# Kernel optimization log

Hardware: AMD Instinct MI355X
Metric: run time of the kernel (lower is better)

The kernel has to match this reference:

```python
import jax, jax.numpy as jnp
import numpy as np


def setup_inputs() -> dict:
    key = jax.random.key(0)
    k1, k2 = jax.random.split(key)
    B, Sx, Sy, D = 8, 2048, 2048, 1024
    x = jax.random.normal(k1, (B, Sx, D), dtype=jnp.float32)
    y = jax.random.normal(k2, (B, Sy, D), dtype=jnp.float32)
    return {"x": x, "y": y}


def reference(x, y):
    # e[b,i,j] = x[b,i,:] . y[b,j,:]  (UNscaled, as in the original)
    e = jnp.einsum('bid,bjd->bij', x, y)
    ai = jax.nn.softmax(e, axis=-1)
    # a[b,i,:] = sum_j ai[b,i,j] * y[b,j,:]
    a = jnp.einsum('bij,bjd->bid', ai, y)
    # concat along feature dim; dropout p=0 -> identity
    out = jnp.concatenate([x, a], axis=-1)  # [B, Sx, 2D]
    return out
```

## Files before the change

kernel.cpp:

```cpp
#include <hip/hip_runtime.h>
#include <stdint.h>

#define SX 2048
#define SYY 2048
#define DDIM 1024
#define NBATCH 8

typedef _Float16 f16;
typedef __attribute__((ext_vector_type(2))) _Float16 h2_t;
typedef __attribute__((ext_vector_type(4))) _Float16 h4_t;
typedef __attribute__((ext_vector_type(8))) _Float16 h8_t;
typedef __attribute__((ext_vector_type(4))) float fx4_t;

__device__ __forceinline__ void gload_lds16(const void* g, void* l) {
  __builtin_amdgcn_global_load_lds((const __attribute__((address_space(1))) void*)g,
                                   (__attribute__((address_space(3))) void*)l,
                                   16, 0, 0);
}

__global__ __launch_bounds__(256) void k_prep_x(const float4* __restrict__ x,
                                                float* __restrict__ out,
                                                h4_t* __restrict__ x16, long n4) {
  long i = (long)blockIdx.x * blockDim.x + threadIdx.x;
  long stride = (long)gridDim.x * blockDim.x;
  for (; i < n4; i += stride) {
    long bi = i >> 8;
    int dq = (int)(i & 255);
    float4 v = x[i];
    *(float4*)(out + bi * (2 * DDIM) + dq * 4) = v;
    h4_t h = { (f16)v.x, (f16)v.y, (f16)v.z, (f16)v.w };
    x16[i] = h;
  }
}

__global__ __launch_bounds__(256) void k_trans(const float* __restrict__ y,
                                               f16* __restrict__ y16,
                                               f16* __restrict__ yt16) {
  __shared__ f16 tile[64][72];
  int z = blockIdx.z;
  int d0 = blockIdx.x * 64, j0 = blockIdx.y * 64;
  const float* yb = y + (size_t)z * SYY * DDIM;
  f16* y16b = y16 + (size_t)z * SYY * DDIM;
  f16* ytb = yt16 + (size_t)z * DDIM * SYY;
  int t = threadIdx.x;
  int jl = t >> 2;
  int dq = t & 3;
#pragma unroll
  for (int s = 0; s < 4; ++s) {
    int dl = dq * 16 + s * 4;
    float4 v = *(const float4*)(yb + (size_t)(j0 + jl) * DDIM + d0 + dl);
    h4_t h = { (f16)v.x, (f16)v.y, (f16)v.z, (f16)v.w };
    *(h4_t*)(y16b + (size_t)(j0 + jl) * DDIM + d0 + dl) = h;
    *(h4_t*)&tile[jl][dl] = h;
  }
  __syncthreads();
  int dl2 = t >> 2;
  int jq = t & 3;
  f16 vbuf[16] __attribute__((aligned(16)));
#pragma unroll
  for (int u = 0; u < 16; ++u) vbuf[u] = tile[jq * 16 + u][dl2];
  f16* orow = ytb + (size_t)(d0 + dl2) * SYY + j0 + jq * 16;
  *(uint4*)orow = *(const uint4*)&vbuf[0];
  *(uint4*)(orow + 8) = *(const uint4*)&vbuf[8];
}

#define PH_BAR() __builtin_amdgcn_s_barrier()

#define STAGE_A(SLOT, HALF, T) {                                               \
    const f16* s_ = aRow + (size_t)((HALF) * 64) * lda + (T) * 64;             \
    f16* d_ = lds + (SLOT) * 8192 + dstoff;                                    \
    gload_lds16(s_, d_);                                                       \
    gload_lds16(s_ + (size_t)128 * lda, d_ + 4096); }

#define STAGE_B(SLOT, HALF, T) {                                               \
    const f16* s_ = bRow + (size_t)((HALF) * 32) * ldb + (T) * 64;             \
    f16* d_ = lds + (SLOT) * 8192 + dstoff;                                    \
    gload_lds16(s_, d_);                                                       \
    gload_lds16(s_ + (size_t)128 * ldb, d_ + 4096); }

#define RD_A(PTR, CB) { _Pragma("unroll") for (int i_ = 0; i_ < 4; ++i_) {     \
    af[i_][0] = *(const h8_t*)((PTR) + (CB) + i_ * 2048 + kb0);                \
    af[i_][1] = *(const h8_t*)((PTR) + (CB) + i_ * 2048 + kb1); } }

#define RD_A_S(PTR, CB, MOFF) { _Pragma("unroll") for (int i_ = 0; i_ < 4; ++i_) { \
    h8_t a0 = *(const h8_t*)((PTR) + (CB) + i_ * 2048 + kb0);                  \
    h8_t a1 = *(const h8_t*)((PTR) + (CB) + i_ * 2048 + kb1);                  \
    h2_t* p0 = (h2_t*)&a0; h2_t* p1 = (h2_t*)&a1;                              \
    _Pragma("unroll") for (int q_ = 0; q_ < 4; ++q_) {                         \
      p0[q_] *= fdc[(MOFF) + i_]; p1[q_] *= fdc[(MOFF) + i_]; }                \
    af[i_][0] = a0; af[i_][1] = a1; } }

#define RD_B(PTR, CB, NH) { _Pragma("unroll") for (int j_ = 0; j_ < 2; ++j_) { \
    bf[(NH) + j_][0] = *(const h8_t*)((PTR) + (CB) + j_ * 2048 + kb0);         \
    bf[(NH) + j_][1] = *(const h8_t*)((PTR) + (CB) + j_ * 2048 + kb1); } }

#define MM(MH, NH) { __builtin_amdgcn_s_setprio(1);                            \
  _Pragma("unroll") for (int i_ = 0; i_ < 4; ++i_)                             \
  _Pragma("unroll") for (int j_ = 0; j_ < 2; ++j_) {                           \
    acc[(MH) + i_][(NH) + j_] = __builtin_amdgcn_mfma_f32_16x16x32_f16(        \
        af[i_][0], bf[(NH) + j_][0], acc[(MH) + i_][(NH) + j_], 0, 0, 0);      \
    acc[(MH) + i_][(NH) + j_] = __builtin_amdgcn_mfma_f32_16x16x32_f16(        \
        af[i_][1], bf[(NH) + j_][1], acc[(MH) + i_][(NH) + j_], 0, 0, 0); }    \
  __builtin_amdgcn_s_setprio(0); }

#define DECODE_TILE()                                                          \
  int bid = blockIdx.x;                                                        \
  int id = bid;                                                                \
  if ((nblk & 7) == 0) { int cpx = nblk >> 3; id = (bid & 7) * cpx + (bid >> 3); } \
  int tpz = ntm * ntn;                                                         \
  int z = id / tpz;                                                            \
  int rem = id - z * tpz;                                                      \
  int mt, ntl;                                                                 \
  if ((ntm & 1) == 0) {                                                        \
    int ht = tpz >> 1, hm = ntm >> 1;                                          \
    int half = rem / ht, j = rem - half * ht;                                  \
    ntl = j / hm; mt = half * hm + (j - ntl * hm);                             \
  } else { mt = rem / ntn; ntl = rem - mt * ntn; }                             \
  int m0 = mt * 256, n0 = ntl * 256;

#define GEMM_COMMON_SETUP()                                                    \
  const int tid = threadIdx.x;                                                 \
  const int lane = tid & 63, w = tid >> 6;                                     \
  const int wr = w >> 2, wc = w & 3;                                           \
  const int fr = lane & 15, fh = lane >> 4;                                    \
  const f16* Ab = A + (size_t)z * a_zs + (size_t)(a_row0 + m0) * lda;          \
  const f16* Bb = B + (size_t)z * b_zs + (size_t)n0 * ldb;                     \
  const int l0 = 8 * w + (lane >> 3);                                          \
  const int r0a = l0;                                                          \
  const int r0b = ((l0 >> 5) << 6) | (l0 & 31);                                \
  const int swz = 8 * ((lane & 7) ^ (lane >> 3));                              \
  const f16* aRow = Ab + (size_t)r0a * lda + swz;                              \
  const f16* bRow = Bb + (size_t)r0b * ldb + swz;                              \
  const int dstoff = w * 512 + lane * 8;                                       \
  const char* ldsAlo = (const char*)lds + wr * 8192 + fr * 128;                \
  const char* ldsAhi = ldsAlo + 16384;                                         \
  const char* ldsBlo = (const char*)lds + 32768 + wc * 4096 + fr * 128;        \
  const char* ldsBhi = ldsBlo + 16384;                                         \
  const int kb0 = ((0 + fh) ^ (fr & 7)) * 16;                                  \
  const int kb1 = ((4 + fh) ^ (fr & 7)) * 16;

__global__ __launch_bounds__(512, 2) void k_gemm1(
    const f16* __restrict__ A, long a_zs, int a_row0, int lda,
    const f16* __restrict__ B, long b_zs, int ldb,
    f16* __restrict__ U, long u_zs,
    float2* __restrict__ ML, int mrows,
    int K, int ntm, int ntn, int nblk)
{
  __shared__ f16 lds[65536];
  DECODE_TILE();
  GEMM_COMMON_SETUP();

  const int nt = K >> 6;
  const int ng = nt >> 1;

  fx4_t acc[8][4];
#pragma unroll
  for (int i = 0; i < 8; ++i)
#pragma unroll
    for (int j = 0; j < 4; ++j) { fx4_t zv = {0.f,0.f,0.f,0.f}; acc[i][j] = zv; }
  h8_t af[4][2], bf[4][2];

  STAGE_A(0, 0, 0); STAGE_A(1, 1, 0); STAGE_B(2, 0, 0); STAGE_B(3, 1, 0);
  STAGE_A(4, 0, 1); STAGE_B(6, 0, 1); STAGE_B(7, 1, 1);
  asm volatile("s_waitcnt vmcnt(6)" ::: "memory");
  PH_BAR();

  for (int g = 0; g < ng; ++g) {
    const int T1 = 2 * g + 1, T2 = 2 * g + 2, T3 = 2 * g + 3;
    const bool nl = (g < ng - 1);
    RD_A(ldsAlo, 0); RD_B(ldsBlo, 0, 0);
    STAGE_A(5, 1, T1);
    PH_BAR();
    MM(0, 0);
    PH_BAR();
    RD_B(ldsBhi, 0, 2);
    if (nl) STAGE_A(0, 0, T2);
    PH_BAR();
    MM(0, 2);
    PH_BAR();
    RD_A(ldsAhi, 0);
    if (nl) STAGE_B(2, 0, T2);
    PH_BAR();
    MM(4, 0);
    PH_BAR();
    if (nl) STAGE_B(3, 1, T2);
    PH_BAR();
    MM(4, 2);
    if (nl) { asm volatile("s_waitcnt vmcnt(6)" ::: "memory"); }
    else    { asm volatile("s_waitcnt vmcnt(0)" ::: "memory"); }
    PH_BAR();
    RD_A(ldsAlo, 65536); RD_B(ldsBlo, 65536, 0);
    if (nl) STAGE_A(1, 1, T2);
    PH_BAR();
    MM(0, 0);
    PH_BAR();
    RD_B(ldsBhi, 65536, 2);
    if (nl) STAGE_A(4, 0, T3);
    PH_BAR();
    MM(0, 2);
    PH_BAR();
    RD_A(ldsAhi, 65536);
    if (nl) STAGE_B(6, 0, T3);
    PH_BAR();
    MM(4, 0);
    PH_BAR();
    if (nl) STAGE_B(7, 1, T3);
    PH_BAR();
    MM(4, 2);
    asm volatile("s_waitcnt vmcnt(6)" ::: "memory");
    PH_BAR();
  }

  __syncthreads();
  float* red = (float*)lds;
  const int rbase = wr * 128 + fh * 4;
  float pm[8][4];
#pragma unroll
  for (int mi = 0; mi < 8; ++mi)
#pragma unroll
    for (int rr = 0; rr < 4; ++rr)
      pm[mi][rr] = fmaxf(fmaxf(acc[mi][0][rr], acc[mi][1][rr]),
                         fmaxf(acc[mi][2][rr], acc[mi][3][rr]));
#pragma unroll
  for (int off = 8; off > 0; off >>= 1)
#pragma unroll
    for (int mi = 0; mi < 8; ++mi)
#pragma unroll
      for (int rr = 0; rr < 4; ++rr)
        pm[mi][rr] = fmaxf(pm[mi][rr], __shfl_xor(pm[mi][rr], off));
  if (fr == 0)
#pragma unroll
    for (int mi = 0; mi < 8; ++mi)
#pragma unroll
      for (int rr = 0; rr < 4; ++rr)
        red[wc * 256 + rbase + mi * 16 + rr] = pm[mi][rr];
  __syncthreads();
  float mrow[8][4];
#pragma unroll
  for (int mi = 0; mi < 8; ++mi)
#pragma unroll
    for (int rr = 0; rr < 4; ++rr) {
      int r = rbase + mi * 16 + rr;
      mrow[mi][rr] = fmaxf(fmaxf(red[r], red[256 + r]),
                           fmaxf(red[512 + r], red[768 + r]));
    }
  __syncthreads();
  float ps[8][4];
#pragma unroll
  for (int mi = 0; mi < 8; ++mi)
#pragma unroll
    for (int rr = 0; rr < 4; ++rr) {
      float s = 0.f;
#pragma unroll
      for (int ni = 0; ni < 4; ++ni) {
        float e = __expf(acc[mi][ni][rr] - mrow[mi][rr]);
        acc[mi][ni][rr] = e;
        s += e;
      }
      ps[mi][rr] = s;
    }
#pragma unroll
  for (int off = 8; off > 0; off >>= 1)
#pragma unroll
    for (int mi = 0; mi < 8; ++mi)
#pragma unroll
      for (int rr = 0; rr < 4; ++rr)
        ps[mi][rr] += __shfl_xor(ps[mi][rr], off);
  if (fr == 0)
#pragma unroll
    for (int mi = 0; mi < 8; ++mi)
#pragma unroll
      for (int rr = 0; rr < 4; ++rr)
        red[wc * 256 + rbase + mi * 16 + rr] = ps[mi][rr];
  __syncthreads();
  f16* Ub = U + (size_t)z * u_zs;
#pragma unroll
  for (int mi = 0; mi < 8; ++mi)
#pragma unroll
    for (int ni = 0; ni < 4; ++ni)
#pragma unroll
      for (int rr = 0; rr < 4; ++rr)
        Ub[(size_t)(m0 + rbase + mi * 16 + rr) * SYY +
           n0 + wc * 64 + ni * 16 + fr] = (f16)acc[mi][ni][rr];
  if (wc == 0 && fr == 0) {
    float2* MLp = ML + ((size_t)z * 8 + ntl) * mrows + m0;
#pragma unroll
    for (int mi = 0; mi < 8; ++mi)
#pragma unroll
      for (int rr = 0; rr < 4; ++rr) {
        int r = rbase + mi * 16 + rr;
        float l4 = red[r] + red[256 + r] + red[512 + r] + red[768 + r];
        float2 v; v.x = mrow[mi][rr]; v.y = l4;
        MLp[r] = v;
      }
  }
}

__global__ __launch_bounds__(256) void k_mlred(const float2* __restrict__ ML,
                                               f16* __restrict__ Fq,
                                               int rows, long total) {
  long idx = (long)blockIdx.x * blockDim.x + threadIdx.x;
  if (idx >= total) return;
  int z = (int)(idx / rows);
  int r = (int)(idx - (long)z * rows);
  float2 v[8];
  float M = -3.4e38f;
#pragma unroll
  for (int t = 0; t < 8; ++t) {
    v[t] = ML[((size_t)z * 8 + t) * rows + r];
    M = fmaxf(M, v[t].x);
  }
  float L = 0.f;
#pragma unroll
  for (int t = 0; t < 8; ++t) L += v[t].y * __expf(v[t].x - M);
  float inv = 1.0f / L;
#pragma unroll
  for (int t = 0; t < 8; ++t)
    Fq[((size_t)z * 8 + t) * rows + r] = (f16)(__expf(v[t].x - M) * inv);
}

__global__ __launch_bounds__(512, 2) void k_gemm2(
    const f16* __restrict__ A, long a_zs, int a_row0, int lda,
    const f16* __restrict__ B, long b_zs, int ldb,
    float* __restrict__ C, long c_zs, int c_row0, int ldc, int c_col0,
    const f16* __restrict__ Fq, int mrows,
    int K, int ntm, int ntn, int nblk)
{
  __shared__ f16 lds[65536];
  DECODE_TILE();
  GEMM_COMMON_SETUP();

  const int nt = K >> 6;
  const int ng = nt >> 1;

  fx4_t acc[8][4];
#pragma unroll
  for (int i = 0; i < 8; ++i)
#pragma unroll
    for (int j = 0; j < 4; ++j) { fx4_t zv = {0.f,0.f,0.f,0.f}; acc[i][j] = zv; }
  h8_t af[4][2], bf[4][2];

  const f16* Fb = Fq + (size_t)z * 8 * mrows + m0 + wr * 128 + fr;
  h2_t fdc[8], fdn[8];
#pragma unroll
  for (int i = 0; i < 8; ++i) {
    f16 fv = Fb[i * 16];
    h2_t d; d[0] = fv; d[1] = fv; fdn[i] = d;
  }

  STAGE_A(0, 0, 0); STAGE_A(1, 1, 0); STAGE_B(2, 0, 0); STAGE_B(3, 1, 0);
  STAGE_A(4, 0, 1); STAGE_B(6, 0, 1); STAGE_B(7, 1, 1);
  asm volatile("s_waitcnt vmcnt(6)" ::: "memory");
  PH_BAR();

  for (int g = 0; g < ng; ++g) {
    const int T1 = 2 * g + 1, T2 = 2 * g + 2, T3 = 2 * g + 3;
    const bool nl = (g < ng - 1);
    if ((g & 1) == 0) {
#pragma unroll
      for (int i = 0; i < 8; ++i) fdc[i] = fdn[i];
      int tn = (g >> 1) + 1;
      if (tn < 8) {
        const f16* Fn = Fb + (size_t)tn * mrows;
#pragma unroll
        for (int i = 0; i < 8; ++i) {
          f16 fv = Fn[i * 16];
          h2_t d; d[0] = fv; d[1] = fv; fdn[i] = d;
        }
      }
    }
    RD_A_S(ldsAlo, 0, 0); RD_B(ldsBlo, 0, 0);
    STAGE_A(5, 1, T1);
    PH_BAR();
    MM(0, 0);
    PH_BAR();
    RD_B(ldsBhi, 0, 2);
    if (nl) STAGE_A(0, 0, T2);
    PH_BAR();
    MM(0, 2);
    PH_BAR();
    RD_A_S(ldsAhi, 0, 4);
    if (nl) STAGE_B(2, 0, T2);
    PH_BAR();
    MM(4, 0);
    PH_BAR();
    if (nl) STAGE_B(3, 1, T2);
    PH_BAR();
    MM(4, 2);
    if (nl) { asm volatile("s_waitcnt vmcnt(6)" ::: "memory"); }
    else    { asm volatile("s_waitcnt vmcnt(0)" ::: "memory"); }
    PH_BAR();
    RD_A_S(ldsAlo, 65536, 0); RD_B(ldsBlo, 65536, 0);
    if (nl) STAGE_A(1, 1, T2);
    PH_BAR();
    MM(0, 0);
    PH_BAR();
    RD_B(ldsBhi, 65536, 2);
    if (nl) STAGE_A(4, 0, T3);
    PH_BAR();
    MM(0, 2);
    PH_BAR();
    RD_A_S(ldsAhi, 65536, 4);
    if (nl) STAGE_B(6, 0, T3);
    PH_BAR();
    MM(4, 0);
    PH_BAR();
    if (nl) STAGE_B(7, 1, T3);
    PH_BAR();
    MM(4, 2);
    asm volatile("s_waitcnt vmcnt(6)" ::: "memory");
    PH_BAR();
  }

  float* Cb = C + (size_t)z * c_zs +
              (size_t)(c_row0 + m0 + wr * 128) * ldc + c_col0 + n0 + wc * 64;
#pragma unroll
  for (int mi = 0; mi < 8; ++mi)
#pragma unroll
    for (int ni = 0; ni < 4; ++ni)
#pragma unroll
      for (int r = 0; r < 4; ++r)
        Cb[(size_t)(mi * 16 + fh * 4 + r) * ldc + ni * 16 + fr] = acc[mi][ni][r];
}

extern "C" void kernel_launch(void* const* d_in, const int* in_sizes, int n_in,
                              void* d_out, int out_size, void* d_ws, size_t ws_size,
                              hipStream_t stream) {
  (void)in_sizes; (void)n_in; (void)out_size;
  const float* x = (const float*)d_in[0];
  const float* y = (const float*)d_in[1];
  float* out = (float*)d_out;

  size_t per_batch = (size_t)SX * SYY * 2 + (size_t)8 * SX * 8 + (size_t)8 * SX * 2 +
                     (size_t)SX * DDIM * 2 + (size_t)SYY * DDIM * 2 +
                     (size_t)DDIM * SYY * 2;
  int nb = (int)(ws_size / per_batch);
  if (nb > NBATCH) nb = NBATCH;
  int CH = SX;
  if (nb < 1) {
    nb = 1;
    size_t conv = (size_t)SX * DDIM * 2 + (size_t)SYY * DDIM * 2 +
                  (size_t)DDIM * SYY * 2;
    size_t avail = ws_size > conv ? ws_size - conv : 0;
    long ch = (long)(avail / ((size_t)SYY * 2 + 80));
    ch = (ch / 256) * 256;
    if (ch < 256) ch = 256;
    if (ch > SX) ch = SX;
    CH = (int)ch;
  }

  char* w = (char*)d_ws;
  f16* Ubuf = (f16*)w;            size_t off = (size_t)nb * CH * SYY * 2;
  float2* MLbuf = (float2*)(w + off); off += (size_t)nb * 8 * CH * 8;
  f16* Fqbuf = (f16*)(w + off);   off += (size_t)nb * 8 * CH * 2;
  f16* X16 = (f16*)(w + off);     off += (size_t)nb * SX * DDIM * 2;
  f16* Y16 = (f16*)(w + off);     off += (size_t)nb * SYY * DDIM * 2;
  f16* Yt16 = (f16*)(w + off);

  for (int b0 = 0; b0 < NBATCH; b0 += nb) {
    int nbc = (NBATCH - b0 < nb) ? (NBATCH - b0) : nb;
    k_prep_x<<<2048, 256, 0, stream>>>(
        (const float4*)(x + (size_t)b0 * SX * DDIM),
        out + (size_t)b0 * SX * 2 * DDIM, (h4_t*)X16,
        (long)nbc * SX * (DDIM / 4));
    dim3 tg(DDIM / 64, SYY / 64, nbc);
    k_trans<<<tg, 256, 0, stream>>>(y + (size_t)b0 * SYY * DDIM, Y16, Yt16);

    for (int i0 = 0; i0 < SX; i0 += CH) {
      int ntm = CH / 256;
      int nblk1 = nbc * ntm * (SYY / 256);
      k_gemm1<<<nblk1, 512, 0, stream>>>(X16, (long)SX * DDIM, i0, DDIM,
                                         Y16, (long)SYY * DDIM, DDIM,
                                         Ubuf, (long)CH * SYY,
                                         MLbuf, CH,
                                         DDIM, ntm, SYY / 256, nblk1);
      long rows_total = (long)nbc * CH;
      k_mlred<<<(unsigned)((rows_total + 255) / 256), 256, 0, stream>>>(
          MLbuf, Fqbuf, CH, rows_total);
      int nblk2 = nbc * ntm * (DDIM / 256);
      k_gemm2<<<nblk2, 512, 0, stream>>>(Ubuf, (long)CH * SYY, 0, SYY,
                                         Yt16, (long)DDIM * SYY, SYY,
                                         out + (size_t)b0 * SX * 2 * DDIM,
                                         (long)SX * 2 * DDIM, i0, 2 * DDIM, DDIM,
                                         Fqbuf, CH,
                                         SYY, ntm, DDIM / 256, nblk2);
    }
  }
}
```

Baseline: 221.0 us.

## Process two tiles per gemm1 block, prefetching the next tile during epilogue

k_gemm1 now launches half as many blocks, each computing two output tiles back to back. The global-to-LDS staging for the second tile starts while the first tile's last k-steps and softmax epilogue run, so the prologue and epilogue are hidden inside one continuous pipeline. The epilogue is also restructured: the per-row max and sum are found with in-wave shuffles and one LDS exchange in a separate region, replacing several __syncthreads rounds. In k_gemm2 the scale-factor prefetch load moves to mid-iteration. The costs are larger LDS, more index arithmetic, fewer blocks to spread across CUs, and a more complex pipeline.

```diff
diff --git a/kernel.cpp b/kernel.cpp
--- a/kernel.cpp
+++ b/kernel.cpp
@@ -66,14 +66,14 @@
 
 #define PH_BAR() __builtin_amdgcn_s_barrier()
 
-#define STAGE_A(SLOT, HALF, T) {                                               \
-    const f16* s_ = aRow + (size_t)((HALF) * 64) * lda + (T) * 64;             \
+#define STAGE_A(AR, SLOT, HALF, T) {                                           \
+    const f16* s_ = (AR) + (size_t)((HALF) * 64) * lda + (T) * 64;             \
     f16* d_ = lds + (SLOT) * 8192 + dstoff;                                    \
     gload_lds16(s_, d_);                                                       \
     gload_lds16(s_ + (size_t)128 * lda, d_ + 4096); }
 
-#define STAGE_B(SLOT, HALF, T) {                                               \
-    const f16* s_ = bRow + (size_t)((HALF) * 32) * ldb + (T) * 64;             \
+#define STAGE_B(BR, SLOT, HALF, T) {                                           \
+    const f16* s_ = (BR) + (size_t)((HALF) * 32) * ldb + (T) * 64;             \
     f16* d_ = lds + (SLOT) * 8192 + dstoff;                                    \
     gload_lds16(s_, d_);                                                       \
     gload_lds16(s_ + (size_t)128 * ldb, d_ + 4096); }
@@ -103,34 +103,14 @@
         af[i_][1], bf[(NH) + j_][1], acc[(MH) + i_][(NH) + j_], 0, 0, 0); }    \
   __builtin_amdgcn_s_setprio(0); }
 
-#define DECODE_TILE()                                                          \
-  int bid = blockIdx.x;                                                        \
-  int id = bid;                                                                \
-  if ((nblk & 7) == 0) { int cpx = nblk >> 3; id = (bid & 7) * cpx + (bid >> 3); } \
-  int tpz = ntm * ntn;                                                         \
-  int z = id / tpz;                                                            \
-  int rem = id - z * tpz;                                                      \
-  int mt, ntl;                                                                 \
-  if ((ntm & 1) == 0) {                                                        \
-    int ht = tpz >> 1, hm = ntm >> 1;                                          \
-    int half = rem / ht, j = rem - half * ht;                                  \
-    ntl = j / hm; mt = half * hm + (j - ntl * hm);                             \
-  } else { mt = rem / ntn; ntl = rem - mt * ntn; }                             \
-  int m0 = mt * 256, n0 = ntl * 256;
-
 #define GEMM_COMMON_SETUP()                                                    \
   const int tid = threadIdx.x;                                                 \
   const int lane = tid & 63, w = tid >> 6;                                     \
   const int wr = w >> 2, wc = w & 3;                                           \
   const int fr = lane & 15, fh = lane >> 4;                                    \
-  const f16* Ab = A + (size_t)z * a_zs + (size_t)(a_row0 + m0) * lda;          \
-  const f16* Bb = B + (size_t)z * b_zs + (size_t)n0 * ldb;                     \
   const int l0 = 8 * w + (lane >> 3);                                          \
-  const int r0a = l0;                                                          \
   const int r0b = ((l0 >> 5) << 6) | (l0 & 31);                                \
   const int swz = 8 * ((lane & 7) ^ (lane >> 3));                              \
-  const f16* aRow = Ab + (size_t)r0a * lda + swz;                              \
-  const f16* bRow = Bb + (size_t)r0b * ldb + swz;                              \
   const int dstoff = w * 512 + lane * 8;                                       \
   const char* ldsAlo = (const char*)lds + wr * 8192 + fr * 128;                \
   const char* ldsAhi = ldsAlo + 16384;                                         \
@@ -139,19 +119,44 @@
   const int kb0 = ((0 + fh) ^ (fr & 7)) * 16;                                  \
   const int kb1 = ((4 + fh) ^ (fr & 7)) * 16;
 
+#define COMPUTE_TILE(IDX, AR, BR, ZV, M0V, N0V) {                              \
+    int id_ = (IDX);                                                           \
+    ZV = id_ / tpz; int rem_ = id_ - ZV * tpz;                                 \
+    int mt_, ntl_;                                                             \
+    if ((ntm & 1) == 0) {                                                      \
+      int ht_ = tpz >> 1, hm_ = ntm >> 1;                                      \
+      int half_ = rem_ / ht_, j_ = rem_ - half_ * ht_;                         \
+      ntl_ = j_ / hm_; mt_ = half_ * hm_ + (j_ - ntl_ * hm_);                  \
+    } else { mt_ = rem_ / ntn; ntl_ = rem_ - mt_ * ntn; }                      \
+    M0V = mt_ * 256; N0V = ntl_ * 256;                                         \
+    AR = A + (size_t)ZV * a_zs + (size_t)(a_row0 + M0V) * lda                  \
+           + (size_t)l0 * lda + swz;                                           \
+    BR = B + (size_t)ZV * b_zs + (size_t)N0V * ldb                             \
+           + (size_t)r0b * ldb + swz; }
+
 __global__ __launch_bounds__(512, 2) void k_gemm1(
     const f16* __restrict__ A, long a_zs, int a_row0, int lda,
     const f16* __restrict__ B, long b_zs, int ldb,
     f16* __restrict__ U, long u_zs,
     float2* __restrict__ ML, int mrows,
-    int K, int ntm, int ntn, int nblk)
+    int K, int ntm, int ntn, int nblk, int tpb)
 {
-  __shared__ f16 lds[65536];
-  DECODE_TILE();
+  __shared__ f16 lds[69632];
   GEMM_COMMON_SETUP();
-
+  const int tpz = ntm * ntn;
   const int nt = K >> 6;
   const int ng = nt >> 1;
+  const int nphys = nblk / tpb;
+  const int nper = nblk >> 3, bper = nphys >> 3;
+  const int xcd = blockIdx.x & 7, lb = blockIdx.x >> 3;
+  const bool chunk8 = ((nblk & 7) == 0) && ((nphys & 7) == 0);
+
+  const f16 *aRowC, *bRowC, *aRowN = A, *bRowN = B;
+  int zC, m0C, n0C, zN = 0, m0N = 0, n0N = 0;
+  int id0 = chunk8 ? (xcd * nper + lb) : (int)blockIdx.x;
+  int idstep = chunk8 ? bper : nphys;
+  COMPUTE_TILE(id0, aRowC, bRowC, zC, m0C, n0C);
+  if (tpb > 1) COMPUTE_TILE(id0 + idstep, aRowN, bRowN, zN, m0N, n0N);
 
   fx4_t acc[8][4];
 #pragma unroll
@@ -160,139 +165,108 @@
     for (int j = 0; j < 4; ++j) { fx4_t zv = {0.f,0.f,0.f,0.f}; acc[i][j] = zv; }
   h8_t af[4][2], bf[4][2];
 
-  STAGE_A(0, 0, 0); STAGE_A(1, 1, 0); STAGE_B(2, 0, 0); STAGE_B(3, 1, 0);
-  STAGE_A(4, 0, 1); STAGE_B(6, 0, 1); STAGE_B(7, 1, 1);
+  STAGE_A(aRowC, 0, 0, 0); STAGE_A(aRowC, 1, 1, 0);
+  STAGE_B(bRowC, 2, 0, 0); STAGE_B(bRowC, 3, 1, 0);
+  STAGE_A(aRowC, 4, 0, 1); STAGE_B(bRowC, 6, 0, 1); STAGE_B(bRowC, 7, 1, 1);
   asm volatile("s_waitcnt vmcnt(6)" ::: "memory");
   PH_BAR();
 
-  for (int g = 0; g < ng; ++g) {
-    const int T1 = 2 * g + 1, T2 = 2 * g + 2, T3 = 2 * g + 3;
-    const bool nl = (g < ng - 1);
+  const int GG = ng * tpb, KT = nt * tpb;
+  int tl = 0;
+  for (int gg = 0; gg < GG; ++gg) {
+    const int gloc = gg - tl * ng;
+    const int T1 = 2 * gloc + 1;
+    const int kt2 = 2 * gg + 2, kt3 = 2 * gg + 3;
+    const bool h2 = kt2 < KT, h3 = kt3 < KT;
+    const int tb = (tl + 1) * nt;
+    const bool n2 = kt2 >= tb, n3 = kt3 >= tb;
+    const f16* a2 = n2 ? aRowN : aRowC; const f16* b2 = n2 ? bRowN : bRowC;
+    const f16* a3 = n3 ? aRowN : aRowC; const f16* b3 = n3 ? bRowN : bRowC;
+    const int T2 = kt2 - (n2 ? tb : tl * nt);
+    const int T3 = kt3 - (n3 ? tb : tl * nt);
     RD_A(ldsAlo, 0); RD_B(ldsBlo, 0, 0);
-    STAGE_A(5, 1, T1);
-    PH_BAR();
-    MM(0, 0);
-    PH_BAR();
+    STAGE_A(aRowC, 5, 1, T1);
+    PH_BAR(); MM(0, 0); PH_BAR();
     RD_B(ldsBhi, 0, 2);
-    if (nl) STAGE_A(0, 0, T2);
-    PH_BAR();
-    MM(0, 2);
-    PH_BAR();
+    if (h2) STAGE_A(a2, 0, 0, T2);
+    PH_BAR(); MM(0, 2); PH_BAR();
     RD_A(ldsAhi, 0);
-    if (nl) STAGE_B(2, 0, T2);
-    PH_BAR();
-    MM(4, 0);
-    PH_BAR();
-    if (nl) STAGE_B(3, 1, T2);
-    PH_BAR();
-    MM(4, 2);
-    if (nl) { asm volatile("s_waitcnt vmcnt(6)" ::: "memory"); }
+    if (h2) STAGE_B(b2, 2, 0, T2);
+    PH_BAR(); MM(4, 0); PH_BAR();
+    if (h2) STAGE_B(b2, 3, 1, T2);
+    PH_BAR(); MM(4, 2);
+    if (h2) { asm volatile("s_waitcnt vmcnt(6)" ::: "memory"); }
     else    { asm volatile("s_waitcnt vmcnt(0)" ::: "memory"); }
     PH_BAR();
     RD_A(ldsAlo, 65536); RD_B(ldsBlo, 65536, 0);
-    if (nl) STAGE_A(1, 1, T2);
+    if (h2) STAGE_A(a2, 1, 1, T2);
+    PH_BAR(); MM(0, 0); PH_BAR();
+    RD_B(ldsBhi, 65536, 2);
+    if (h3) STAGE_A(a3, 4, 0, T3);
+    PH_BAR(); MM(0, 2); PH_BAR();
+    RD_A(ldsAhi, 65536);
+    if (h3) STAGE_B(b3, 6, 0, T3);
+    PH_BAR(); MM(4, 0); PH_BAR();
+    if (h3) STAGE_B(b3, 7, 1, T3);
+    PH_BAR(); MM(4, 2);
+    if (h2) { asm volatile("s_waitcnt vmcnt(6)" ::: "memory"); }
+    else    { asm volatile("s_waitcnt vmcnt(0)" ::: "memory"); }
     PH_BAR();
-    MM(0, 0);
-    PH_BAR();
-    RD_B(ldsBhi, 65536, 2);
-    if (nl) STAGE_A(4, 0, T3);
-    PH_BAR();
-    MM(0, 2);
-    PH_BAR();
-    RD_A(ldsAhi, 65536);
-    if (nl) STAGE_B(6, 0, T3);
-    PH_BAR();
-    MM(4, 0);
-    PH_BAR();
-    if (nl) STAGE_B(7, 1, T3);
-    PH_BAR();
-    MM(4, 2);
-    asm volatile("s_waitcnt vmcnt(6)" ::: "memory");
-    PH_BAR();
-  }
-
-  __syncthreads();
-  float* red = (float*)lds;
-  const int rbase = wr * 128 + fh * 4;
-  float pm[8][4];
-#pragma unroll
-  for (int mi = 0; mi < 8; ++mi)
-#pragma unroll
-    for (int rr = 0; rr < 4; ++rr)
-      pm[mi][rr] = fmaxf(fmaxf(acc[mi][0][rr], acc[mi][1][rr]),
-                         fmaxf(acc[mi][2][rr], acc[mi][3][rr]));
-#pragma unroll
-  for (int off = 8; off > 0; off >>= 1)
-#pragma unroll
-    for (int mi = 0; mi < 8; ++mi)
-#pragma unroll
-      for (int rr = 0; rr < 4; ++rr)
-        pm[mi][rr] = fmaxf(pm[mi][rr], __shfl_xor(pm[mi][rr], off));
-  if (fr == 0)
-#pragma unroll
-    for (int mi = 0; mi < 8; ++mi)
-#pragma unroll
-      for (int rr = 0; rr < 4; ++rr)
-        red[wc * 256 + rbase + mi * 16 + rr] = pm[mi][rr];
-  __syncthreads();
-  float mrow[8][4];
-#pragma unroll
-  for (int mi = 0; mi < 8; ++mi)
-#pragma unroll
-    for (int rr = 0; rr < 4; ++rr) {
-      int r = rbase + mi * 16 + rr;
-      mrow[mi][rr] = fmaxf(fmaxf(red[r], red[256 + r]),
-                           fmaxf(red[512 + r], red[768 + r]));
+
+    if (gloc == ng - 1) {
+      float2* mlx = (float2*)(lds + 65536);
+      const int rbase = wr * 128 + fh * 4;
+      float mw[8][4];
+#pragma unroll
+      for (int mi = 0; mi < 8; ++mi)
+#pragma unroll
+        for (int rr = 0; rr < 4; ++rr) {
+          float am = fmaxf(fmaxf(acc[mi][0][rr], acc[mi][1][rr]),
+                           fmaxf(acc[mi][2][rr], acc[mi][3][rr]));
+          am = fmaxf(am, __shfl_xor(am, 1)); am = fmaxf(am, __shfl_xor(am, 2));
+          am = fmaxf(am, __shfl_xor(am, 4)); am = fmaxf(am, __shfl_xor(am, 8));
+          float s = 0.f;
+#pragma unroll
+          for (int ni = 0; ni < 4; ++ni) {
+            float e = __expf(acc[mi][ni][rr] - am);
+            acc[mi][ni][rr] = e; s += e;
+          }
+          s += __shfl_xor(s, 1); s += __shfl_xor(s, 2);
+          s += __shfl_xor(s, 4); s += __shfl_xor(s, 8);
+          mw[mi][rr] = am;
+          if (fr == 0) {
+            float2 v; v.x = am; v.y = s;
+            mlx[(rbase + mi * 16 + rr) * 4 + wc] = v;
+          }
+        }
+      asm volatile("s_waitcnt lgkmcnt(0)" ::: "memory");
+      PH_BAR();
+      f16* Ub = U + (size_t)zC * u_zs;
+      float2* MLp = ML + ((size_t)zC * 8 + (n0C >> 8)) * mrows + m0C;
+#pragma unroll
+      for (int mi = 0; mi < 8; ++mi)
+#pragma unroll
+        for (int rr = 0; rr < 4; ++rr) {
+          int row = rbase + mi * 16 + rr;
+          float4 p01 = *(float4*)&mlx[row * 4 + 0];
+          float4 p23 = *(float4*)&mlx[row * 4 + 2];
+          float mt = fmaxf(fmaxf(p01.x, p01.z), fmaxf(p23.x, p23.z));
+          float lt = p01.y * __expf(p01.x - mt) + p01.w * __expf(p01.z - mt) +
+                     p23.y * __expf(p23.x - mt) + p23.w * __expf(p23.z - mt);
+          float sc = __expf(mw[mi][rr] - mt);
+#pragma unroll
+          for (int ni = 0; ni < 4; ++ni)
+            Ub[(size_t)(m0C + row) * SYY + n0C + wc * 64 + ni * 16 + fr] =
+                (f16)(acc[mi][ni][rr] * sc);
+          if (wc == 0 && fr == 0) { float2 v; v.x = mt; v.y = lt; MLp[row] = v; }
+        }
+      aRowC = aRowN; bRowC = bRowN; zC = zN; m0C = m0N; n0C = n0N;
+      ++tl;
+#pragma unroll
+      for (int i = 0; i < 8; ++i)
+#pragma unroll
+        for (int j = 0; j < 4; ++j) { fx4_t zv = {0.f,0.f,0.f,0.f}; acc[i][j] = zv; }
     }
-  __syncthreads();
-  float ps[8][4];
-#pragma unroll
-  for (int mi = 0; mi < 8; ++mi)
-#pragma unroll
-    for (int rr = 0; rr < 4; ++rr) {
-      float s = 0.f;
-#pragma unroll
-      for (int ni = 0; ni < 4; ++ni) {
-        float e = __expf(acc[mi][ni][rr] - mrow[mi][rr]);
-        acc[mi][ni][rr] = e;
-        s += e;
-      }
-      ps[mi][rr] = s;
-    }
-#pragma unroll
-  for (int off = 8; off > 0; off >>= 1)
-#pragma unroll
-    for (int mi = 0; mi < 8; ++mi)
-#pragma unroll
-      for (int rr = 0; rr < 4; ++rr)
-        ps[mi][rr] += __shfl_xor(ps[mi][rr], off);
-  if (fr == 0)
-#pragma unroll
-    for (int mi = 0; mi < 8; ++mi)
-#pragma unroll
-      for (int rr = 0; rr < 4; ++rr)
-        red[wc * 256 + rbase + mi * 16 + rr] = ps[mi][rr];
-  __syncthreads();
-  f16* Ub = U + (size_t)z * u_zs;
-#pragma unroll
-  for (int mi = 0; mi < 8; ++mi)
-#pragma unroll
-    for (int ni = 0; ni < 4; ++ni)
-#pragma unroll
-      for (int rr = 0; rr < 4; ++rr)
-        Ub[(size_t)(m0 + rbase + mi * 16 + rr) * SYY +
-           n0 + wc * 64 + ni * 16 + fr] = (f16)acc[mi][ni][rr];
-  if (wc == 0 && fr == 0) {
-    float2* MLp = ML + ((size_t)z * 8 + ntl) * mrows + m0;
-#pragma unroll
-    for (int mi = 0; mi < 8; ++mi)
-#pragma unroll
-      for (int rr = 0; rr < 4; ++rr) {
-        int r = rbase + mi * 16 + rr;
-        float l4 = red[r] + red[256 + r] + red[512 + r] + red[768 + r];
-        float2 v; v.x = mrow[mi][rr]; v.y = l4;
-        MLp[r] = v;
-      }
   }
 }
 
@@ -327,8 +301,14 @@
     int K, int ntm, int ntn, int nblk)
 {
   __shared__ f16 lds[65536];
-  DECODE_TILE();
   GEMM_COMMON_SETUP();
+  const int tpz = ntm * ntn;
+  int bid = blockIdx.x;
+  int id = bid;
+  if ((nblk & 7) == 0) { int cpx = nblk >> 3; id = (bid & 7) * cpx + (bid >> 3); }
+  const f16 *aRow, *bRow;
+  int z, m0, n0;
+  COMPUTE_TILE(id, aRow, bRow, z, m0, n0);
 
   const int nt = K >> 6;
   const int ng = nt >> 1;
@@ -348,17 +328,36 @@
     h2_t d; d[0] = fv; d[1] = fv; fdn[i] = d;
   }
 
-  STAGE_A(0, 0, 0); STAGE_A(1, 1, 0); STAGE_B(2, 0, 0); STAGE_B(3, 1, 0);
-  STAGE_A(4, 0, 1); STAGE_B(6, 0, 1); STAGE_B(7, 1, 1);
+  STAGE_A(aRow, 0, 0, 0); STAGE_A(aRow, 1, 1, 0);
+  STAGE_B(bRow, 2, 0, 0); STAGE_B(bRow, 3, 1, 0);
+  STAGE_A(aRow, 4, 0, 1); STAGE_B(bRow, 6, 0, 1); STAGE_B(bRow, 7, 1, 1);
   asm volatile("s_waitcnt vmcnt(6)" ::: "memory");
   PH_BAR();
 
   for (int g = 0; g < ng; ++g) {
     const int T1 = 2 * g + 1, T2 = 2 * g + 2, T3 = 2 * g + 3;
     const bool nl = (g < ng - 1);
-    if ((g & 1) == 0) {
+    const bool ev = ((g & 1) == 0);
+    if (ev) {
 #pragma unroll
       for (int i = 0; i < 8; ++i) fdc[i] = fdn[i];
+    }
+    RD_A_S(ldsAlo, 0, 0); RD_B(ldsBlo, 0, 0);
+    STAGE_A(aRow, 5, 1, T1);
+    PH_BAR(); MM(0, 0); PH_BAR();
+    RD_B(ldsBhi, 0, 2);
+    if (nl) STAGE_A(aRow, 0, 0, T2);
+    PH_BAR(); MM(0, 2); PH_BAR();
+    RD_A_S(ldsAhi, 0, 4);
+    if (nl) STAGE_B(bRow, 2, 0, T2);
+    PH_BAR(); MM(4, 0); PH_BAR();
+    if (nl) STAGE_B(bRow, 3, 1, T2);
+    PH_BAR(); MM(4, 2);
+    if (nl) { asm volatile("s_waitcnt vmcnt(6)" ::: "memory"); }
+    else    { asm volatile("s_waitcnt vmcnt(0)" ::: "memory"); }
+    PH_BAR();
+    RD_A_S(ldsAlo, 65536, 0); RD_B(ldsBlo, 65536, 0);
+    if (ev) {
       int tn = (g >> 1) + 1;
       if (tn < 8) {
         const f16* Fn = Fb + (size_t)tn * mrows;
@@ -369,45 +368,16 @@
         }
       }
     }
-    RD_A_S(ldsAlo, 0, 0); RD_B(ldsBlo, 0, 0);
-    STAGE_A(5, 1, T1);
-    PH_BAR();
-    MM(0, 0);
-    PH_BAR();
-    RD_B(ldsBhi, 0, 2);
-    if (nl) STAGE_A(0, 0, T2);
-    PH_BAR();
-    MM(0, 2);
-    PH_BAR();
-    RD_A_S(ldsAhi, 0, 4);
-    if (nl) STAGE_B(2, 0, T2);
-    PH_BAR();
-    MM(4, 0);
-    PH_BAR();
-    if (nl) STAGE_B(3, 1, T2);
-    PH_BAR();
-    MM(4, 2);
-    if (nl) { asm volatile("s_waitcnt vmcnt(6)" ::: "memory"); }
-    else    { asm volatile("s_waitcnt vmcnt(0)" ::: "memory"); }
-    PH_BAR();
-    RD_A_S(ldsAlo, 65536, 0); RD_B(ldsBlo, 65536, 0);
-    if (nl) STAGE_A(1, 1, T2);
-    PH_BAR();
-    MM(0, 0);
-    PH_BAR();
+    if (nl) STAGE_A(aRow, 1, 1, T2);
+    PH_BAR(); MM(0, 0); PH_BAR();
     RD_B(ldsBhi, 65536, 2);
-    if (nl) STAGE_A(4, 0, T3);
-    PH_BAR();
-    MM(0, 2);
-    PH_BAR();
+    if (nl) STAGE_A(aRow, 4, 0, T3);
+    PH_BAR(); MM(0, 2); PH_BAR();
     RD_A_S(ldsAhi, 65536, 4);
-    if (nl) STAGE_B(6, 0, T3);
-    PH_BAR();
-    MM(4, 0);
-    PH_BAR();
-    if (nl) STAGE_B(7, 1, T3);
-    PH_BAR();
-    MM(4, 2);
+    if (nl) STAGE_B(bRow, 6, 0, T3);
+    PH_BAR(); MM(4, 0); PH_BAR();
+    if (nl) STAGE_B(bRow, 7, 1, T3);
+    PH_BAR(); MM(4, 2);
     asm volatile("s_waitcnt vmcnt(6)" ::: "memory");
     PH_BAR();
   }
@@ -469,11 +439,13 @@
     for (int i0 = 0; i0 < SX; i0 += CH) {
       int ntm = CH / 256;
       int nblk1 = nbc * ntm * (SYY / 256);
-      k_gemm1<<<nblk1, 512, 0, stream>>>(X16, (long)SX * DDIM, i0, DDIM,
-                                         Y16, (long)SYY * DDIM, DDIM,
-                                         Ubuf, (long)CH * SYY,
-                                         MLbuf, CH,
-                                         DDIM, ntm, SYY / 256, nblk1);
+      int tpb = ((nblk1 & 15) == 0) ? 2 : 1;
+      int nphys1 = nblk1 / tpb;
+      k_gemm1<<<nphys1, 512, 0, stream>>>(X16, (long)SX * DDIM, i0, DDIM,
+                                          Y16, (long)SYY * DDIM, DDIM,
+                                          Ubuf, (long)CH * SYY,
+                                          MLbuf, CH,
+                                          DDIM, ntm, SYY / 256, nblk1, tpb);
       long rows_total = (long)nbc * CH;
       k_mlred<<<(unsigned)((rows_total + 255) / 256), 256, 0, stream>>>(
           MLbuf, Fqbuf, CH, rows_total);
```

Measured after the change: 235.5 us. 1.07x slower.

## Fuse softmax max/sum reductions per wave and coalesce U stores via LDS

Applied to the files above, without the earlier changes.

The QK epilogue now computes each wave's row max and exp-sum locally with shuffles, then merges the four wave partials through LDS in a single pass using online-softmax rescaling, removing one barrier-separated reduction round. The exponentials are rescaled to the tile-wide max before conversion to f16, staged through LDS, and written to U with 16-byte row-contiguous stores instead of scattered 2-byte stores. The PV kernel also moves the prefetch of the next F scale factors later in the loop so its latency overlaps the first MFMA half. The cost is extra exp calls, an additional LDS round trip, and different rounding of U values.

```diff
diff --git a/kernel.cpp b/kernel.cpp
--- a/kernel.cpp
+++ b/kernel.cpp
@@ -212,88 +212,62 @@
   }
 
   __syncthreads();
-  float* red = (float*)lds;
+  float2* mlx = (float2*)lds;
   const int rbase = wr * 128 + fh * 4;
-  float pm[8][4];
+  float mw[8][4];
 #pragma unroll
   for (int mi = 0; mi < 8; ++mi)
 #pragma unroll
-    for (int rr = 0; rr < 4; ++rr)
-      pm[mi][rr] = fmaxf(fmaxf(acc[mi][0][rr], acc[mi][1][rr]),
-                         fmaxf(acc[mi][2][rr], acc[mi][3][rr]));
-#pragma unroll
-  for (int off = 8; off > 0; off >>= 1)
-#pragma unroll
-    for (int mi = 0; mi < 8; ++mi)
-#pragma unroll
-      for (int rr = 0; rr < 4; ++rr)
-        pm[mi][rr] = fmaxf(pm[mi][rr], __shfl_xor(pm[mi][rr], off));
-  if (fr == 0)
-#pragma unroll
-    for (int mi = 0; mi < 8; ++mi)
-#pragma unroll
-      for (int rr = 0; rr < 4; ++rr)
-        red[wc * 256 + rbase + mi * 16 + rr] = pm[mi][rr];
-  __syncthreads();
-  float mrow[8][4];
-#pragma unroll
-  for (int mi = 0; mi < 8; ++mi)
-#pragma unroll
     for (int rr = 0; rr < 4; ++rr) {
-      int r = rbase + mi * 16 + rr;
-      mrow[mi][rr] = fmaxf(fmaxf(red[r], red[256 + r]),
-                           fmaxf(red[512 + r], red[768 + r]));
+      float am = fmaxf(fmaxf(acc[mi][0][rr], acc[mi][1][rr]),
+                       fmaxf(acc[mi][2][rr], acc[mi][3][rr]));
+      am = fmaxf(am, __shfl_xor(am, 1)); am = fmaxf(am, __shfl_xor(am, 2));
+      am = fmaxf(am, __shfl_xor(am, 4)); am = fmaxf(am, __shfl_xor(am, 8));
+      float s = 0.f;
+#pragma unroll
+      for (int ni = 0; ni < 4; ++ni) {
+        float e = __expf(acc[mi][ni][rr] - am);
+        acc[mi][ni][rr] = e; s += e;
+      }
+      s += __shfl_xor(s, 1); s += __shfl_xor(s, 2);
+      s += __shfl_xor(s, 4); s += __shfl_xor(s, 8);
+      mw[mi][rr] = am;
+      if (fr == 0) {
+        float2 v; v.x = am; v.y = s;
+        mlx[(rbase + mi * 16 + rr) * 4 + wc] = v;
+      }
     }
   __syncthreads();
-  float ps[8][4];
+  float2* MLp = ML + ((size_t)z * 8 + (n0 >> 8)) * mrows + m0;
 #pragma unroll
   for (int mi = 0; mi < 8; ++mi)
 #pragma unroll
     for (int rr = 0; rr < 4; ++rr) {
-      float s = 0.f;
-#pragma unroll
-      for (int ni = 0; ni < 4; ++ni) {
-        float e = __expf(acc[mi][ni][rr] - mrow[mi][rr]);
-        acc[mi][ni][rr] = e;
-        s += e;
-      }
-      ps[mi][rr] = s;
+      int row = rbase + mi * 16 + rr;
+      float4 p01 = *(float4*)&mlx[row * 4 + 0];
+      float4 p23 = *(float4*)&mlx[row * 4 + 2];
+      float mt = fmaxf(fmaxf(p01.x, p01.z), fmaxf(p23.x, p23.z));
+      float lt = p01.y * __expf(p01.x - mt) + p01.w * __expf(p01.z - mt) +
+                 p23.y * __expf(p23.x - mt) + p23.w * __expf(p23.z - mt);
+      if (wc == 0 && fr == 0) { float2 v; v.x = mt; v.y = lt; MLp[row] = v; }
+      mw[mi][rr] = __expf(mw[mi][rr] - mt);
     }
-#pragma unroll
-  for (int off = 8; off > 0; off >>= 1)
-#pragma unroll
-    for (int mi = 0; mi < 8; ++mi)
+  __syncthreads();
+  f16* wreg = lds + w * 8192;
+#pragma unroll
+  for (int mi = 0; mi < 8; ++mi)
+#pragma unroll
+    for (int ni = 0; ni < 4; ++ni)
 #pragma unroll
       for (int rr = 0; rr < 4; ++rr)
-        ps[mi][rr] += __shfl_xor(ps[mi][rr], off);
-  if (fr == 0)
-#pragma unroll
-    for (int mi = 0; mi < 8; ++mi)
-#pragma unroll
-      for (int rr = 0; rr < 4; ++rr)
-        red[wc * 256 + rbase + mi * 16 + rr] = ps[mi][rr];
-  __syncthreads();
-  f16* Ub = U + (size_t)z * u_zs;
-#pragma unroll
-  for (int mi = 0; mi < 8; ++mi)
-#pragma unroll
-    for (int ni = 0; ni < 4; ++ni)
-#pragma unroll
-      for (int rr = 0; rr < 4; ++rr)
-        Ub[(size_t)(m0 + rbase + mi * 16 + rr) * SYY +
-           n0 + wc * 64 + ni * 16 + fr] = (f16)acc[mi][ni][rr];
-  if (wc == 0 && fr == 0) {
-    float2* MLp = ML + ((size_t)z * 8 + ntl) * mrows + m0;
-#pragma unroll
-    for (int mi = 0; mi < 8; ++mi)
-#pragma unroll
-      for (int rr = 0; rr < 4; ++rr) {
-        int r = rbase + mi * 16 + rr;
-        float l4 = red[r] + red[256 + r] + red[512 + r] + red[768 + r];
-        float2 v; v.x = mrow[mi][rr]; v.y = l4;
-        MLp[r] = v;
-      }
-  }
+        wreg[(mi * 16 + fh * 4 + rr) * 64 + ni * 16 + fr] =
+            (f16)(acc[mi][ni][rr] * mw[mi][rr]);
+  f16* Ub = U + (size_t)z * u_zs + (size_t)(m0 + wr * 128 + (lane >> 3)) * SYY +
+            n0 + wc * 64 + (lane & 7) * 8;
+  const f16* rsrc = wreg + (lane >> 3) * 64 + (lane & 7) * 8;
+#pragma unroll
+  for (int i = 0; i < 16; ++i)
+    *(uint4*)(Ub + (size_t)(i * 8) * SYY) = *(const uint4*)(rsrc + i * 512);
 }
 
 __global__ __launch_bounds__(256) void k_mlred(const float2* __restrict__ ML,
@@ -356,9 +330,27 @@
   for (int g = 0; g < ng; ++g) {
     const int T1 = 2 * g + 1, T2 = 2 * g + 2, T3 = 2 * g + 3;
     const bool nl = (g < ng - 1);
-    if ((g & 1) == 0) {
+    const bool ev = ((g & 1) == 0);
+    if (ev) {
 #pragma unroll
       for (int i = 0; i < 8; ++i) fdc[i] = fdn[i];
+    }
+    RD_A_S(ldsAlo, 0, 0); RD_B(ldsBlo, 0, 0);
+    STAGE_A(5, 1, T1);
+    PH_BAR(); MM(0, 0); PH_BAR();
+    RD_B(ldsBhi, 0, 2);
+    if (nl) STAGE_A(0, 0, T2);
+    PH_BAR(); MM(0, 2); PH_BAR();
+    RD_A_S(ldsAhi, 0, 4);
+    if (nl) STAGE_B(2, 0, T2);
+    PH_BAR(); MM(4, 0); PH_BAR();
+    if (nl) STAGE_B(3, 1, T2);
+    PH_BAR(); MM(4, 2);
+    if (nl) { asm volatile("s_waitcnt vmcnt(6)" ::: "memory"); }
+    else    { asm volatile("s_waitcnt vmcnt(0)" ::: "memory"); }
+    PH_BAR();
+    RD_A_S(ldsAlo, 65536, 0); RD_B(ldsBlo, 65536, 0);
+    if (ev) {
       int tn = (g >> 1) + 1;
       if (tn < 8) {
         const f16* Fn = Fb + (size_t)tn * mrows;
@@ -369,45 +361,16 @@
         }
       }
     }
-    RD_A_S(ldsAlo, 0, 0); RD_B(ldsBlo, 0, 0);
-    STAGE_A(5, 1, T1);
-    PH_BAR();
-    MM(0, 0);
-    PH_BAR();
-    RD_B(ldsBhi, 0, 2);
-    if (nl) STAGE_A(0, 0, T2);
-    PH_BAR();
-    MM(0, 2);
-    PH_BAR();
-    RD_A_S(ldsAhi, 0, 4);
-    if (nl) STAGE_B(2, 0, T2);
-    PH_BAR();
-    MM(4, 0);
-    PH_BAR();
-    if (nl) STAGE_B(3, 1, T2);
-    PH_BAR();
-    MM(4, 2);
-    if (nl) { asm volatile("s_waitcnt vmcnt(6)" ::: "memory"); }
-    else    { asm volatile("s_waitcnt vmcnt(0)" ::: "memory"); }
-    PH_BAR();
-    RD_A_S(ldsAlo, 65536, 0); RD_B(ldsBlo, 65536, 0);
     if (nl) STAGE_A(1, 1, T2);
-    PH_BAR();
-    MM(0, 0);
-    PH_BAR();
+    PH_BAR(); MM(0, 0); PH_BAR();
     RD_B(ldsBhi, 65536, 2);
     if (nl) STAGE_A(4, 0, T3);
-    PH_BAR();
-    MM(0, 2);
-    PH_BAR();
+    PH_BAR(); MM(0, 2); PH_BAR();
     RD_A_S(ldsAhi, 65536, 4);
     if (nl) STAGE_B(6, 0, T3);
-    PH_BAR();
-    MM(4, 0);
-    PH_BAR();
+    PH_BAR(); MM(4, 0); PH_BAR();
     if (nl) STAGE_B(7, 1, T3);
-    PH_BAR();
-    MM(4, 2);
+    PH_BAR(); MM(4, 2);
     asm volatile("s_waitcnt vmcnt(6)" ::: "memory");
     PH_BAR();
   }
```

Result: slower. 231.3 us (+4.7%).
